# Performance work log

Measured on AMD Instinct MI355X. Metric: run time of the kernel, lower is better.

## Reference

```python
import jax, jax.numpy as jnp
import numpy as np

N_NODES = 50000
N_EDGES = 800000
IN_FEAT = 256
UNITS = 128
NEG_SLOPE = 0.2  # tf.nn.leaky_relu default alpha


def setup_inputs() -> dict:
    key = jax.random.key(0)
    k1, k2, k3, k4 = jax.random.split(key, 4)
    node_states = jax.random.normal(k1, (N_NODES, IN_FEAT), dtype=jnp.float32)
    edges = jax.random.randint(k2, (N_EDGES, 2), 0, N_NODES, dtype=jnp.int64)
    kernel = jax.random.normal(k3, (IN_FEAT, UNITS), dtype=jnp.float32) * 0.05
    kernel_attention = jax.random.normal(k4, (2 * UNITS, 1), dtype=jnp.float32) * 0.05
    return {"node_states": node_states, "edges": edges,
            "kernel": kernel, "kernel_attention": kernel_attention}


def reference(node_states, edges, kernel, kernel_attention):
    # node_states: [N, F], edges: [E, 2] (col 0 = target/segment, col 1 = source)
    n_nodes = node_states.shape[0]
    tgt = edges[:, 0]
    src = edges[:, 1]

    h = node_states @ kernel  # [N, U]

    # attention score per edge: leaky_relu(concat(h[tgt], h[src]) @ a)
    # split the attention vector so the two matmuls happen per-node (same math,
    # avoids materializing the [E, 2U] concat)
    u = h.shape[1]
    a_tgt = (h @ kernel_attention[:u]).squeeze(-1)  # [N]
    a_src = (h @ kernel_attention[u:]).squeeze(-1)  # [N]
    scores = jax.nn.leaky_relu(a_tgt[tgt] + a_src[src], NEG_SLOPE)  # [E]
    scores = jnp.exp(jnp.clip(scores, -2.0, 2.0))

    # segment softmax over edges grouped by target node
    denom = jax.ops.segment_sum(scores, tgt, num_segments=n_nodes)  # [N]
    attn = scores / denom[tgt]  # [E]

    # weighted aggregation of neighbor features
    out = jax.ops.segment_sum(h[src] * attn[:, None], tgt, num_segments=n_nodes)  # [N, U]
    return out
```

## Files before the change

### kernel.cpp

```cpp
#include <hip/hip_runtime.h>
#include <hip/hip_bf16.h>

#define N_NODES 50000
#define N_EDGES 800000
#define IN_FEAT 256
#define UNITS   128
#define BUCKET  64
#define BIN_SHIFT 8
#define NBINS   196
#define BIN_CAP 4608
#define CHUNK   4096

typedef unsigned short ushort_t;
typedef __bf16 bf16x8 __attribute__((ext_vector_type(8)));
typedef float  f32x4  __attribute__((ext_vector_type(4)));
typedef unsigned short ushort8 __attribute__((ext_vector_type(8)));

__device__ __forceinline__ ushort_t bfbits(float f) {
    __bf16 b = (__bf16)f;
    return __builtin_bit_cast(ushort_t, b);
}

__device__ __forceinline__ void cvt8(const float4& f0, const float4& f1,
                                     ushort_t* dst) {
    bf16x8 u;
    u[0] = (__bf16)f0.x; u[1] = (__bf16)f0.y; u[2] = (__bf16)f0.z; u[3] = (__bf16)f0.w;
    u[4] = (__bf16)f1.x; u[5] = (__bf16)f1.y; u[6] = (__bf16)f1.z; u[7] = (__bf16)f1.w;
    *(bf16x8*)dst = u;
}

__global__ __launch_bounds__(256) void prep_wt_zero(const float* __restrict__ W,
                                                    ushort_t* __restrict__ Wt,
                                                    int* __restrict__ gbin) {
    int i = blockIdx.x * 256 + threadIdx.x;
    if (i < UNITS * IN_FEAT) {
        int n = i >> 8;
        int k = i & 255;
        Wt[i] = bfbits(W[(size_t)k * UNITS + n]);
    }
    if (i < 256) gbin[i] = 0;
}

__global__ __launch_bounds__(256) void gemm_mfma(const float* __restrict__ A,
                                                 const ushort_t* __restrict__ Wt,
                                                 const float* __restrict__ ka,
                                                 ushort_t* __restrict__ Hb,
                                                 float* __restrict__ a_tgt,
                                                 float* __restrict__ a_src, int M) {
    __shared__ __align__(16) ushort_t Bs[128 * 264];
    __shared__ __align__(16) ushort_t As[2 * 64 * 40];
    __shared__ float spt[64][2];
    __shared__ float sps[64][2];
    const int tid  = threadIdx.x;
    const int lane = tid & 63;
    const int wv   = tid >> 6;
    const int wy   = wv >> 1;
    const int wx   = wv & 1;
    const int row0 = blockIdx.x * 64;
    const int quad = lane >> 4;
    const int cl   = lane & 15;

    f32x4 acc[2][4] = {};

#pragma unroll
    for (int t = 0; t < 16; ++t) {
        int j = t * 256 + tid;
        int r = j >> 5;
        int c = (j & 31) * 8;
        *(ushort8*)(Bs + r * 264 + c) = *(const ushort8*)(Wt + r * 256 + c);
    }

    const int ar = tid >> 2, aq = tid & 3;
    const int gr = min(row0 + ar, M - 1);
    const float* aptr = A + (size_t)gr * IN_FEAT + aq * 8;
    ushort_t*    asw  = As + ar * 40 + aq * 8;

    {
        float4 f0 = *(const float4*)(aptr);
        float4 f1 = *(const float4*)(aptr + 4);
        cvt8(f0, f1, asw);
    }
    __syncthreads();

    for (int kc = 0; kc < IN_FEAT; kc += 32) {
        const int cur = (kc >> 5) & 1;
        const bool more = (kc + 32 < IN_FEAT);
        float4 g0, g1;
        if (more) {
            g0 = *(const float4*)(aptr + kc + 32);
            g1 = *(const float4*)(aptr + kc + 36);
        }

        bf16x8 af[2], bff[4];
        const ushort_t* asb = As + cur * 2560;
#pragma unroll
        for (int mi = 0; mi < 2; ++mi)
            af[mi] = *(const bf16x8*)(asb + (wy * 32 + mi * 16 + cl) * 40 + quad * 8);
#pragma unroll
        for (int ni = 0; ni < 4; ++ni)
            bff[ni] = *(const bf16x8*)(Bs + (wx * 64 + ni * 16 + cl) * 264 + kc + quad * 8);
#pragma unroll
        for (int mi = 0; mi < 2; ++mi)
#pragma unroll
            for (int ni = 0; ni < 4; ++ni)
                acc[mi][ni] = __builtin_amdgcn_mfma_f32_16x16x32_bf16(
                    af[mi], bff[ni], acc[mi][ni], 0, 0, 0);

        if (more)
            cvt8(g0, g1, As + (cur ^ 1) * 2560 + ar * 40 + aq * 8);
        __syncthreads();
    }

#pragma unroll
    for (int mi = 0; mi < 2; ++mi) {
#pragma unroll
        for (int ni = 0; ni < 4; ++ni) {
            int col = wx * 64 + ni * 16 + cl;
#pragma unroll
            for (int r = 0; r < 4; ++r) {
                int row = row0 + wy * 32 + mi * 16 + quad * 4 + r;
                if (row < M)
                    Hb[(size_t)row * UNITS + col] = bfbits(acc[mi][ni][r]);
            }
        }
    }

    float kt[4], ks[4];
#pragma unroll
    for (int ni = 0; ni < 4; ++ni) {
        int col = wx * 64 + ni * 16 + cl;
        kt[ni] = ka[col];
        ks[ni] = ka[UNITS + col];
    }
#pragma unroll
    for (int mi = 0; mi < 2; ++mi) {
        float pt[4] = {}, ps[4] = {};
#pragma unroll
        for (int ni = 0; ni < 4; ++ni)
#pragma unroll
            for (int r = 0; r < 4; ++r) {
                pt[r] += acc[mi][ni][r] * kt[ni];
                ps[r] += acc[mi][ni][r] * ks[ni];
            }
#pragma unroll
        for (int r = 0; r < 4; ++r) {
#pragma unroll
            for (int m = 1; m < 16; m <<= 1) {
                pt[r] += __shfl_xor(pt[r], m);
                ps[r] += __shfl_xor(ps[r], m);
            }
            if (cl == 0) {
                int rl = wy * 32 + mi * 16 + quad * 4 + r;
                spt[rl][wx] = pt[r];
                sps[rl][wx] = ps[r];
            }
        }
    }
    __syncthreads();
    if (tid < 64) {
        int row = row0 + tid;
        if (row < M) {
            a_tgt[row] = spt[tid][0] + spt[tid][1];
            a_src[row] = sps[tid][0] + sps[tid][1];
        }
    }
}

__device__ __forceinline__ float edge_score(float at, float as) {
    float s = at + as;
    s = s > 0.f ? s : 0.2f * s;
    s = fminf(fmaxf(s, -2.f), 2.f);
    return __expf(s);
}

__global__ __launch_bounds__(256) void bin_edges(const int* __restrict__ edges,
                                                 int* __restrict__ gbin,
                                                 int2* __restrict__ binbuf, int E) {
    __shared__ int  hist[256];
    __shared__ int  sbase[256];
    __shared__ int  runoff[256];
    __shared__ int  gbase[256];
    __shared__ int  wsum[4];
    __shared__ int2 stage[CHUNK];
    const int tid  = threadIdx.x;
    const int lane = tid & 63, wv = tid >> 6;
    const int e0   = blockIdx.x * CHUNK;

    hist[tid] = 0;
    __syncthreads();

    int2 er[16];
    int  eb[16];
#pragma unroll
    for (int j = 0; j < 16; ++j) {
        int idx = e0 + j * 256 + tid;
        if (idx < E) {
            er[j] = ((const int2*)edges)[idx];
            eb[j] = er[j].x >> BIN_SHIFT;
            atomicAdd(&hist[eb[j]], 1);
        } else eb[j] = -1;
    }
    __syncthreads();

    int h = hist[tid];
    int incl = h;
#pragma unroll
    for (int off = 1; off < 64; off <<= 1) {
        int t = __shfl_up(incl, off);
        if (lane >= off) incl += t;
    }
    if (lane == 63) wsum[wv] = incl;
    __syncthreads();
    int excl = incl - h;
#pragma unroll
    for (int w = 0; w < 4; ++w) if (w < wv) excl += wsum[w];
    sbase[tid]  = excl;
    runoff[tid] = excl;
    __syncthreads();

    if (h > 0) gbase[tid] = atomicAdd(&gbin[tid], h);

#pragma unroll
    for (int j = 0; j < 16; ++j) {
        if (eb[j] >= 0) {
            int p = atomicAdd(&runoff[eb[j]], 1);
            stage[p] = er[j];
        }
    }
    __syncthreads();

    int total = sbase[255] + hist[255];
    for (int p = tid; p < total; p += 256) {
        int2 ts = stage[p];
        int b   = ts.x >> BIN_SHIFT;
        int dst = gbase[b] + (p - sbase[b]);
        if (dst < BIN_CAP)
            binbuf[(size_t)b * BIN_CAP + dst] = ts;
    }
}

__global__ __launch_bounds__(1024) void bucket_scatter(const int2* __restrict__ binbuf,
                                                       const int* __restrict__ gbin,
                                                       const float* __restrict__ at,
                                                       const float* __restrict__ as,
                                                       int* __restrict__ cnt,
                                                       int2* __restrict__ csr, int M) {
    __shared__ int   lcnt[256];
    __shared__ float atl[256];
    const int tid = threadIdx.x;
    const int bin = blockIdx.x;
    const int t0  = bin << BIN_SHIFT;
    if (tid < 256) {
        lcnt[tid] = 0;
        int t = t0 + tid;
        atl[tid] = (t < M) ? at[t] : 0.f;
    }
    __syncthreads();

    const int bcnt = min(gbin[bin], BIN_CAP);
    const int2* src = binbuf + (size_t)bin * BIN_CAP;
    for (int p = tid; p < bcnt; p += 1024) {
        int2 ts = src[p];
        int lt  = ts.x - t0;
        float sc = edge_score(atl[lt], as[ts.y]);
        int r = atomicAdd(&lcnt[lt], 1);
        if (r < BUCKET)
            csr[(size_t)ts.x * BUCKET + r] = make_int2(ts.y, __float_as_int(sc));
    }
    __syncthreads();
    if (tid < 256) {
        int t = t0 + tid;
        if (t < M) cnt[t] = lcnt[tid];
    }
}

__global__ __launch_bounds__(256) void aggregate(const ushort_t* __restrict__ Hb,
                                                 const int* __restrict__ cnt,
                                                 const int2* __restrict__ csr,
                                                 float* __restrict__ out, int M) {
    int wid  = (int)((blockIdx.x * 256 + threadIdx.x) >> 6);
    int lane = threadIdx.x & 63;
    if (wid >= M) return;
    const int g = lane >> 4;
    const int c = lane & 15;
    const int deg = min(cnt[wid], BUCKET);

    int   s_v = 0;
    float w_v = 0.f;
    if (lane < deg) {
        int2 sw = csr[(size_t)wid * BUCKET + lane];
        s_v = sw.x;
        w_v = __int_as_float(sw.y);
    }

    float acc[8] = {};
    int nstep = (deg + 3) >> 2;
#pragma unroll 4
    for (int t = 0; t < nstep; ++t) {
        int slot = t * 4 + g;
        int   src = __shfl(s_v, slot);
        float w   = __shfl(w_v, slot);
        uint4 u = *(const uint4*)(Hb + (size_t)src * UNITS + c * 8);
        acc[0] += w * __uint_as_float(u.x << 16);
        acc[1] += w * __uint_as_float(u.x & 0xffff0000u);
        acc[2] += w * __uint_as_float(u.y << 16);
        acc[3] += w * __uint_as_float(u.y & 0xffff0000u);
        acc[4] += w * __uint_as_float(u.z << 16);
        acc[5] += w * __uint_as_float(u.z & 0xffff0000u);
        acc[6] += w * __uint_as_float(u.w << 16);
        acc[7] += w * __uint_as_float(u.w & 0xffff0000u);
    }

#pragma unroll
    for (int i = 0; i < 8; ++i) {
        acc[i] += __shfl_xor(acc[i], 16);
        acc[i] += __shfl_xor(acc[i], 32);
    }
    float wacc = w_v;
#pragma unroll
    for (int off = 32; off > 0; off >>= 1) wacc += __shfl_xor(wacc, off);
    float scale = (deg > 0) ? 1.0f / wacc : 0.0f;

    if (g == 0) {
        float4 o0 = make_float4(acc[0] * scale, acc[1] * scale,
                                acc[2] * scale, acc[3] * scale);
        float4 o1 = make_float4(acc[4] * scale, acc[5] * scale,
                                acc[6] * scale, acc[7] * scale);
        float* dst = out + (size_t)wid * UNITS + c * 8;
        *(float4*)dst       = o0;
        *(float4*)(dst + 4) = o1;
    }
}

extern "C" void kernel_launch(void* const* d_in, const int* in_sizes, int n_in,
                              void* d_out, int out_size, void* d_ws, size_t ws_size,
                              hipStream_t stream) {
    const float* node_states = (const float*)d_in[0];
    const int*   edges       = (const int*)d_in[1];
    const float* W           = (const float*)d_in[2];
    const float* ka          = (const float*)d_in[3];
    float*       out         = (float*)d_out;

    const int M = N_NODES, E = N_EDGES;

    ushort_t* hb     = (ushort_t*)d_ws;
    float*    a_tgt  = (float*)(hb + (size_t)M * UNITS);
    float*    a_src  = a_tgt + M;
    int*      cnt    = (int*)(a_src + M);
    int*      gbin   = cnt + M;
    int2*     csr    = (int2*)(gbin + 256);
    int2*     binbuf = csr + (size_t)M * BUCKET;
    ushort_t* wt     = (ushort_t*)csr;

    const int nblkA = (E + CHUNK - 1) / CHUNK;

    prep_wt_zero  <<<(UNITS * IN_FEAT + 255) / 256, 256, 0, stream>>>(W, wt, gbin);
    gemm_mfma     <<<(M + 63) / 64, 256, 0, stream>>>(node_states, wt, ka, hb,
                                                      a_tgt, a_src, M);
    bin_edges     <<<nblkA, 256, 0, stream>>>(edges, gbin, binbuf, E);
    bucket_scatter<<<NBINS, 1024, 0, stream>>>(binbuf, gbin, a_tgt, a_src,
                                               cnt, csr, M);
    aggregate     <<<(M * 64 + 255) / 256, 256, 0, stream>>>(hb, cnt, csr, out, M);
}
```

Baseline: 167.7 us.

## Fuse bucket scatter and aggregation, keeping per-node edge buckets in LDS

Merges the bucket_scatter and aggregate kernels into one kernel. Each 1024-thread block builds its 256 nodes' edge lists (source index plus score) in a 128 KB shared-memory bucket array, then its 16 waves each aggregate 16 nodes serially. This removes the global CSR and count arrays, their write/read round trip, and one kernel launch. In exchange, the feature gather now runs on only 196 blocks with large LDS use, which cuts parallelism and the latency hiding that the separate per-node-wave aggregate kernel had.

```diff
diff --git a/kernel.cpp b/kernel.cpp
--- a/kernel.cpp
+++ b/kernel.cpp
@@ -239,12 +239,11 @@
     }
 }
 
-__global__ __launch_bounds__(1024) void bucket_scatter(const int2* __restrict__ binbuf,
-                                                       const int* __restrict__ gbin,
-                                                       const float* __restrict__ at,
-                                                       const float* __restrict__ as,
-                                                       int* __restrict__ cnt,
-                                                       int2* __restrict__ csr, int M) {
+__global__ __launch_bounds__(1024) void scatter_aggregate(
+        const int2* __restrict__ binbuf, const int* __restrict__ gbin,
+        const float* __restrict__ at, const float* __restrict__ as,
+        const ushort_t* __restrict__ Hb, float* __restrict__ out, int M) {
+    __shared__ int2  bucket[256 * BUCKET];
     __shared__ int   lcnt[256];
     __shared__ float atl[256];
     const int tid = threadIdx.x;
@@ -265,70 +264,66 @@
         float sc = edge_score(atl[lt], as[ts.y]);
         int r = atomicAdd(&lcnt[lt], 1);
         if (r < BUCKET)
-            csr[(size_t)ts.x * BUCKET + r] = make_int2(ts.y, __float_as_int(sc));
-    }
-    __syncthreads();
-    if (tid < 256) {
-        int t = t0 + tid;
-        if (t < M) cnt[t] = lcnt[tid];
-    }
-}
-
-__global__ __launch_bounds__(256) void aggregate(const ushort_t* __restrict__ Hb,
-                                                 const int* __restrict__ cnt,
-                                                 const int2* __restrict__ csr,
-                                                 float* __restrict__ out, int M) {
-    int wid  = (int)((blockIdx.x * 256 + threadIdx.x) >> 6);
-    int lane = threadIdx.x & 63;
-    if (wid >= M) return;
-    const int g = lane >> 4;
-    const int c = lane & 15;
-    const int deg = min(cnt[wid], BUCKET);
-
-    int   s_v = 0;
-    float w_v = 0.f;
-    if (lane < deg) {
-        int2 sw = csr[(size_t)wid * BUCKET + lane];
-        s_v = sw.x;
-        w_v = __int_as_float(sw.y);
-    }
-
-    float acc[8] = {};
-    int nstep = (deg + 3) >> 2;
+            bucket[(lt << 6) + r] = make_int2(ts.y, __float_as_int(sc));
+    }
+    __syncthreads();
+
+    const int lane = tid & 63;
+    const int wv   = tid >> 6;
+    const int g    = lane >> 4;
+    const int c    = lane & 15;
+
+    for (int ln = 0; ln < 16; ++ln) {
+        const int lt  = wv * 16 + ln;
+        const int node = t0 + lt;
+        if (node >= M) break;
+        const int deg = min(lcnt[lt], BUCKET);
+
+        int   s_v = 0;
+        float w_v = 0.f;
+        if (lane < deg) {
+            int2 sw = bucket[(lt << 6) + lane];
+            s_v = sw.x;
+            w_v = __int_as_float(sw.y);
+        }
+
+        float acc[8] = {};
+        int nstep = (deg + 3) >> 2;
 #pragma unroll 4
-    for (int t = 0; t < nstep; ++t) {
-        int slot = t * 4 + g;
-        int   src = __shfl(s_v, slot);
-        float w   = __shfl(w_v, slot);
-        uint4 u = *(const uint4*)(Hb + (size_t)src * UNITS + c * 8);
-        acc[0] += w * __uint_as_float(u.x << 16);
-        acc[1] += w * __uint_as_float(u.x & 0xffff0000u);
-        acc[2] += w * __uint_as_float(u.y << 16);
-        acc[3] += w * __uint_as_float(u.y & 0xffff0000u);
-        acc[4] += w * __uint_as_float(u.z << 16);
-        acc[5] += w * __uint_as_float(u.z & 0xffff0000u);
-        acc[6] += w * __uint_as_float(u.w << 16);
-        acc[7] += w * __uint_as_float(u.w & 0xffff0000u);
-    }
-
-#pragma unroll
-    for (int i = 0; i < 8; ++i) {
-        acc[i] += __shfl_xor(acc[i], 16);
-        acc[i] += __shfl_xor(acc[i], 32);
-    }
-    float wacc = w_v;
-#pragma unroll
-    for (int off = 32; off > 0; off >>= 1) wacc += __shfl_xor(wacc, off);
-    float scale = (deg > 0) ? 1.0f / wacc : 0.0f;
-
-    if (g == 0) {
-        float4 o0 = make_float4(acc[0] * scale, acc[1] * scale,
-                                acc[2] * scale, acc[3] * scale);
-        float4 o1 = make_float4(acc[4] * scale, acc[5] * scale,
-                                acc[6] * scale, acc[7] * scale);
-        float* dst = out + (size_t)wid * UNITS + c * 8;
-        *(float4*)dst       = o0;
-        *(float4*)(dst + 4) = o1;
+        for (int t = 0; t < nstep; ++t) {
+            int slot = t * 4 + g;
+            int   srcn = __shfl(s_v, slot);
+            float w    = __shfl(w_v, slot);
+            uint4 u = *(const uint4*)(Hb + (size_t)srcn * UNITS + c * 8);
+            acc[0] += w * __uint_as_float(u.x << 16);
+            acc[1] += w * __uint_as_float(u.x & 0xffff0000u);
+            acc[2] += w * __uint_as_float(u.y << 16);
+            acc[3] += w * __uint_as_float(u.y & 0xffff0000u);
+            acc[4] += w * __uint_as_float(u.z << 16);
+            acc[5] += w * __uint_as_float(u.z & 0xffff0000u);
+            acc[6] += w * __uint_as_float(u.w << 16);
+            acc[7] += w * __uint_as_float(u.w & 0xffff0000u);
+        }
+
+#pragma unroll
+        for (int i = 0; i < 8; ++i) {
+            acc[i] += __shfl_xor(acc[i], 16);
+            acc[i] += __shfl_xor(acc[i], 32);
+        }
+        float wacc = w_v;
+#pragma unroll
+        for (int off = 32; off > 0; off >>= 1) wacc += __shfl_xor(wacc, off);
+        float scale = (deg > 0) ? 1.0f / wacc : 0.0f;
+
+        if (g == 0) {
+            float4 o0 = make_float4(acc[0] * scale, acc[1] * scale,
+                                    acc[2] * scale, acc[3] * scale);
+            float4 o1 = make_float4(acc[4] * scale, acc[5] * scale,
+                                    acc[6] * scale, acc[7] * scale);
+            float* dst = out + (size_t)node * UNITS + c * 8;
+            *(float4*)dst       = o0;
+            *(float4*)(dst + 4) = o1;
+        }
     }
 }
 
@@ -346,19 +341,16 @@
     ushort_t* hb     = (ushort_t*)d_ws;
     float*    a_tgt  = (float*)(hb + (size_t)M * UNITS);
     float*    a_src  = a_tgt + M;
-    int*      cnt    = (int*)(a_src + M);
-    int*      gbin   = cnt + M;
-    int2*     csr    = (int2*)(gbin + 256);
-    int2*     binbuf = csr + (size_t)M * BUCKET;
-    ushort_t* wt     = (ushort_t*)csr;
+    int*      gbin   = (int*)(a_src + M);
+    int2*     binbuf = (int2*)(gbin + 256);
+    ushort_t* wt     = (ushort_t*)binbuf;
 
     const int nblkA = (E + CHUNK - 1) / CHUNK;
 
-    prep_wt_zero  <<<(UNITS * IN_FEAT + 255) / 256, 256, 0, stream>>>(W, wt, gbin);
-    gemm_mfma     <<<(M + 63) / 64, 256, 0, stream>>>(node_states, wt, ka, hb,
-                                                      a_tgt, a_src, M);
-    bin_edges     <<<nblkA, 256, 0, stream>>>(edges, gbin, binbuf, E);
-    bucket_scatter<<<NBINS, 1024, 0, stream>>>(binbuf, gbin, a_tgt, a_src,
-                                               cnt, csr, M);
-    aggregate     <<<(M * 64 + 255) / 256, 256, 0, stream>>>(hb, cnt, csr, out, M);
-}
+    prep_wt_zero    <<<(UNITS * IN_FEAT + 255) / 256, 256, 0, stream>>>(W, wt, gbin);
+    gemm_mfma       <<<(M + 63) / 64, 256, 0, stream>>>(node_states, wt, ka, hb,
+                                                        a_tgt, a_src, M);
+    bin_edges       <<<nblkA, 256, 0, stream>>>(edges, gbin, binbuf, E);
+    scatter_aggregate<<<NBINS, 1024, 0, stream>>>(binbuf, gbin, a_tgt, a_src,
+                                                  hb, out, M);
+}
```

Result: slower. 174.7 us (+4.2%).
